# Optimization experiments

Measured on AMD Instinct MI355X. Metric: run time of the kernel, lower is better.

The kernel has to match this reference:

```python
import jax, jax.numpy as jnp
import numpy as np

D_MODEL = 1024
N_HEADS = 16
D_HEAD = D_MODEL // N_HEADS
RANK = 256
N_COMPRESS = 64
N_EXPAND = 64
N_KNOWLEDGE = 4096
K_COMPRESS = 16
K_EXPAND = 8
K_KNOW = 8


def setup_inputs() -> dict:
    key = jax.random.key(0)
    ks = jax.random.split(key, 13)
    B, S = 8, 1024
    x = jax.random.normal(ks[0], (B, S, D_MODEL), dtype=jnp.float32)
    u = jax.random.uniform(ks[1], (B, S), dtype=jnp.float32)
    importance = u / jnp.sum(u, axis=-1, keepdims=True)  # token importance weights
    s = 0.02
    compress_w = jax.random.normal(ks[2], (N_COMPRESS, D_MODEL)) * s
    expQ_w = jax.random.normal(ks[3], (N_EXPAND, D_MODEL)) * s
    expK_w = jax.random.normal(ks[4], (N_EXPAND, D_MODEL)) * s
    expV_w = jax.random.normal(ks[5], (N_EXPAND, D_MODEL)) * s
    memory_w = jax.random.normal(ks[6], (N_COMPRESS, D_MODEL)) * s
    compress_neurons = jax.random.normal(ks[7], (N_COMPRESS, D_MODEL, RANK)) / jnp.sqrt(D_MODEL)
    expand_pool = jax.random.normal(ks[8], (N_EXPAND, RANK, D_MODEL)) / jnp.sqrt(RANK)
    knowledge_K = jax.random.normal(ks[9], (N_KNOWLEDGE, RANK)) * s
    knowledge_V = jax.random.normal(ks[10], (N_KNOWLEDGE, D_MODEL)) * s
    Wo = jax.random.normal(ks[11], (D_MODEL, D_MODEL)) / jnp.sqrt(D_MODEL)
    return dict(x=x, importance=importance, compress_w=compress_w, expQ_w=expQ_w,
                expK_w=expK_w, expV_w=expV_w, memory_w=memory_w,
                compress_neurons=compress_neurons, expand_pool=expand_pool,
                knowledge_K=knowledge_K, knowledge_V=knowledge_V, Wo=Wo)


def _route(x, importance, w_lin, k):
    # softmax router pref [B,S,N], importance-weighted sum -> [B,N], renorm, top-k renorm
    pref = jax.nn.softmax(jnp.einsum('bsd,nd->bsn', x, w_lin), axis=-1)
    w = jnp.einsum('bs,bsn->bn', importance, pref)
    w = w / (jnp.sum(w, axis=-1, keepdims=True) + 1e-8)
    tw, ti = jax.lax.top_k(w, k)
    tw = tw / (jnp.sum(tw, axis=-1, keepdims=True) + 1e-8)
    return tw, ti


def _forward(x, importance, compress_w, expQ_w, expK_w, expV_w, memory_w,
             compress_neurons, expand_pool, knowledge_K, knowledge_V, Wo):
    B, S, D = x.shape
    # ---- attention routing ----
    cw, ci = _route(x, importance, compress_w, K_COMPRESS)
    shared_c = jnp.einsum('bk,bkdr->bdr', cw, compress_neurons[ci])  # [B,D,R]
    h = jnp.einsum('bsd,bdr->bsr', x, shared_c)                      # [B,S,R]

    def expand(w_lin):
        ew, ei = _route(x, importance, w_lin, K_EXPAND)
        shared = jnp.einsum('bk,bkrd->brd', ew, expand_pool[ei])     # [B,R,D]
        return jnp.einsum('bsr,brd->bsd', h, shared)                 # [B,S,D]

    Q, K, V = expand(expQ_w), expand(expK_w), expand(expV_w)
    Qh = Q.reshape(B, S, N_HEADS, D_HEAD).transpose(0, 2, 1, 3)
    Kh = K.reshape(B, S, N_HEADS, D_HEAD).transpose(0, 2, 1, 3)
    Vh = V.reshape(B, S, N_HEADS, D_HEAD).transpose(0, 2, 1, 3)
    scores = jnp.einsum('bhqd,bhkd->bhqk', Qh, Kh) / jnp.sqrt(jnp.float32(D_HEAD))
    causal = jnp.tril(jnp.ones((S, S), dtype=bool))
    scores = jnp.where(causal, scores, jnp.float32(-1e30))
    attn = jax.nn.softmax(scores, axis=-1)
    out = jnp.einsum('bhqk,bhkd->bhqd', attn, Vh)
    out = out.transpose(0, 2, 1, 3).reshape(B, S, D)
    attn_out = jnp.einsum('bsd,ed->bse', out, Wo)

    # ---- memory routing (knowledge lookup) ----
    mw, mi = _route(x, importance, memory_w, K_COMPRESS)
    shared_m = jnp.einsum('bk,bkdr->bdr', mw, compress_neurons[mi])
    hm = jnp.einsum('bsd,bdr->bsr', x, shared_m)                     # [B,S,R]
    kscores = jnp.einsum('bsr,nr->bsn', hm, knowledge_K) / jnp.sqrt(jnp.float32(RANK))
    top_s, top_i = jax.lax.top_k(kscores, K_KNOW)                    # [B,S,k]
    p = jax.nn.softmax(top_s, axis=-1)
    mem_out = jnp.einsum('bsk,bskd->bsd', p, knowledge_V[top_i])

    return attn_out + mem_out


def reference(x, importance, compress_w, expQ_w, expK_w, expV_w, memory_w,
              compress_neurons, expand_pool, knowledge_K, knowledge_V, Wo):
    return _forward(x, importance, compress_w, expQ_w, expK_w, expV_w, memory_w,
                    compress_neurons, expand_pool, knowledge_K, knowledge_V, Wo)
```

## Files before the change

kernel.cpp:

```cpp
#include <hip/hip_runtime.h>

#define Bn   8
#define Sn   1024
#define Dn   1024
#define Rn   256
#define NHn  16
#define DHn  64
#define NKn  4096
#define TOK  (Bn*Sn)
#define EPE  (Dn*Rn)

typedef __attribute__((ext_vector_type(8))) short short8;
typedef __attribute__((ext_vector_type(4))) float f32x4;
typedef __attribute__((ext_vector_type(4))) unsigned short ushort4v;

__device__ inline unsigned short f2bf(float f) {
    union { float f; unsigned u; } v; v.f = f;
    unsigned r = v.u + 0x7fffu + ((v.u >> 16) & 1u);
    return (unsigned short)(r >> 16);
}
__device__ inline float bf2f(unsigned short h) {
    union { unsigned u; float f; } v; v.u = ((unsigned)h) << 16;
    return v.f;
}
__device__ inline void f2bf_split(float f, unsigned short& hi, unsigned short& lo) {
    hi = f2bf(f);
    lo = f2bf(f - bf2f(hi));
}

__global__ __launch_bounds__(256) void convert_split(
    const float* __restrict__ src, unsigned short* __restrict__ hi,
    unsigned short* __restrict__ lo, long long n4)
{
    long long i = (long long)blockIdx.x*256 + threadIdx.x;
    if (i >= n4) return;
    float4 f = *(const float4*)&src[i*4];
    float vals[4] = {f.x, f.y, f.z, f.w};
    ushort4v h, l;
#pragma unroll
    for (int e = 0; e < 4; ++e) {
        unsigned short a, b2; f2bf_split(vals[e], a, b2);
        h[e] = a; l[e] = b2;
    }
    *(ushort4v*)&hi[i*4] = h;
    *(ushort4v*)&lo[i*4] = l;
}

__global__ __launch_bounds__(256) void gemm_pre(
    const unsigned short* __restrict__ Ahi, const unsigned short* __restrict__ Alo,
    const unsigned short* __restrict__ Bhi, const unsigned short* __restrict__ Blo,
    void* __restrict__ C0, void* __restrict__ C1,
    int M, int N, int K, long long sA, long long sB, long long sC,
    float alpha, int bTrans, int passes, int outMode)
{
    Ahi += (size_t)blockIdx.z * sA;
    if (Alo) Alo += (size_t)blockIdx.z * sA;
    Bhi += (size_t)blockIdx.z * sB;
    if (Blo) Blo += (size_t)blockIdx.z * sB;
    __shared__ __align__(16) unsigned short AsH[128][40];
    __shared__ __align__(16) unsigned short AsL[128][40];
    __shared__ __align__(16) unsigned short BsH[64][40];
    __shared__ __align__(16) unsigned short BsL[64][40];
    int tid = threadIdx.x;
    int wave = tid >> 6, lane = tid & 63;
    int lr = lane & 15, lg = lane >> 4;
    int wm = (wave >> 1)*64, wn = (wave & 1)*32;
    int row0 = blockIdx.y*128, col0 = blockIdx.x*64;

    f32x4 acc[4][2];
#pragma unroll
    for (int i = 0; i < 4; ++i)
#pragma unroll
        for (int j = 0; j < 2; ++j) acc[i][j] = (f32x4){0.f,0.f,0.f,0.f};

    for (int k0 = 0; k0 < K; k0 += 32) {
        __syncthreads();
#pragma unroll
        for (int g = 0; g < 2; ++g) {
            int idx = tid + g*256;
            int m2 = idx >> 2, kk = (idx & 3)*8;
            size_t so = (size_t)(row0 + m2)*K + k0 + kk;
            *(short8*)&AsH[m2][kk] = *(const short8*)&Ahi[so];
            if (passes >= 2) *(short8*)&AsL[m2][kk] = *(const short8*)&Alo[so];
        }
        if (!bTrans) {
            int n2 = tid >> 2, kk = (tid & 3)*8;
            size_t so = (size_t)(col0 + n2)*K + k0 + kk;
            *(short8*)&BsH[n2][kk] = *(const short8*)&Bhi[so];
            if (passes >= 3) *(short8*)&BsL[n2][kk] = *(const short8*)&Blo[so];
        } else {
            int kk = tid >> 3, n0 = (tid & 7)*8;
            size_t so = (size_t)(k0 + kk)*N + col0 + n0;
            short8 wh = *(const short8*)&Bhi[so];
#pragma unroll
            for (int e = 0; e < 8; ++e) BsH[n0+e][kk] = (unsigned short)wh[e];
            if (passes >= 3) {
                short8 wl = *(const short8*)&Blo[so];
#pragma unroll
                for (int e = 0; e < 8; ++e) BsL[n0+e][kk] = (unsigned short)wl[e];
            }
        }
        __syncthreads();
        short8 afH[4], bfH[2];
#pragma unroll
        for (int i = 0; i < 4; ++i) afH[i] = *(const short8*)&AsH[wm + i*16 + lr][lg*8];
#pragma unroll
        for (int j = 0; j < 2; ++j) bfH[j] = *(const short8*)&BsH[wn + j*16 + lr][lg*8];
#pragma unroll
        for (int i = 0; i < 4; ++i)
#pragma unroll
            for (int j = 0; j < 2; ++j)
                acc[i][j] = __builtin_amdgcn_mfma_f32_16x16x32_bf16(afH[i], bfH[j], acc[i][j], 0, 0, 0);
        if (passes >= 2) {
            short8 afL[4];
#pragma unroll
            for (int i = 0; i < 4; ++i) afL[i] = *(const short8*)&AsL[wm + i*16 + lr][lg*8];
#pragma unroll
            for (int i = 0; i < 4; ++i)
#pragma unroll
                for (int j = 0; j < 2; ++j)
                    acc[i][j] = __builtin_amdgcn_mfma_f32_16x16x32_bf16(afL[i], bfH[j], acc[i][j], 0, 0, 0);
        }
        if (passes >= 3) {
            short8 bfL[2];
#pragma unroll
            for (int j = 0; j < 2; ++j) bfL[j] = *(const short8*)&BsL[wn + j*16 + lr][lg*8];
#pragma unroll
            for (int i = 0; i < 4; ++i)
#pragma unroll
                for (int j = 0; j < 2; ++j)
                    acc[i][j] = __builtin_amdgcn_mfma_f32_16x16x32_bf16(afH[i], bfL[j], acc[i][j], 0, 0, 0);
        }
    }
#pragma unroll
    for (int i = 0; i < 4; ++i)
#pragma unroll
        for (int j = 0; j < 2; ++j)
#pragma unroll
            for (int r = 0; r < 4; ++r) {
                size_t eo = (size_t)(row0 + wm + i*16 + lg*4 + r)*N + col0 + wn + j*16 + lr;
                float val = acc[i][j][r] * alpha;
                if (outMode == 0) {
                    ((float*)C0 + (size_t)blockIdx.z*sC)[eo] = val;
                } else if (outMode == 1) {
                    ((unsigned short*)C0 + (size_t)blockIdx.z*sC)[eo] = f2bf(val);
                } else if (outMode == 2) {
                    unsigned short h, l; f2bf_split(val, h, l);
                    ((unsigned short*)C0 + (size_t)blockIdx.z*sC)[eo] = h;
                    ((unsigned short*)C1 + (size_t)blockIdx.z*sC)[eo] = l;
                } else {
                    ((float*)C0 + (size_t)blockIdx.z*sC)[eo] = val;
                    ((unsigned short*)C1 + (size_t)blockIdx.z*sC)[eo] = f2bf(val);
                }
            }
}

__global__ __launch_bounds__(256) void router_post(
    const float* __restrict__ logits, const float* __restrict__ imp,
    float* __restrict__ partial)
{
    int blk = blockIdx.x;
    int chunk = blk & 3, b = (blk >> 2) & 7, r = blk >> 5;
    int tid = threadIdx.x, lane = tid & 63, wv = tid >> 6;
    float acc = 0.f;
    for (int i = wv; i < 256; i += 4) {
        int t = b*1024 + chunk*256 + i;
        float lgv = logits[(size_t)t*320 + r*64 + lane];
        float mx = lgv;
        for (int off = 32; off >= 1; off >>= 1) mx = fmaxf(mx, __shfl_xor(mx, off));
        float e = __expf(lgv - mx);
        float s = e;
        for (int off = 32; off >= 1; off >>= 1) s += __shfl_xor(s, off);
        acc += imp[t] * e / s;
    }
    __shared__ float red[4][64];
    red[wv][lane] = acc;
    __syncthreads();
    if (tid < 64)
        partial[((size_t)(r*8 + b)*4 + chunk)*64 + tid]
            = red[0][tid] + red[1][tid] + red[2][tid] + red[3][tid];
}

__global__ void topk_router(const float* __restrict__ partial,
                            float* __restrict__ tw, int* __restrict__ ti)
{
    int rb = blockIdx.x;
    int r  = rb >> 3;
    int lane = threadIdx.x;
    float v = partial[((size_t)rb*4 + 0)*64 + lane] + partial[((size_t)rb*4 + 1)*64 + lane]
            + partial[((size_t)rb*4 + 2)*64 + lane] + partial[((size_t)rb*4 + 3)*64 + lane];
    float s = v;
    for (int off = 32; off >= 1; off >>= 1) s += __shfl_xor(s, off);
    v = v / (s + 1e-8f);
    int k = (r == 0 || r == 4) ? 16 : 8;
    __shared__ float tv[16];
    __shared__ int   tix[16];
    float cur = v;
    for (int it = 0; it < k; ++it) {
        float bv = cur; int bi = lane;
        for (int off = 32; off >= 1; off >>= 1) {
            float ov = __shfl_xor(bv, off);
            int   oi = __shfl_xor(bi, off);
            if (ov > bv || (ov == bv && oi < bi)) { bv = ov; bi = oi; }
        }
        if (bi == lane) cur = -1e30f;
        if (lane == 0) { tv[it] = bv; tix[it] = bi; }
    }
    __syncthreads();
    float s2 = 0.f;
    for (int i = 0; i < k; ++i) s2 += tv[i];
    float inv = 1.f / (s2 + 1e-8f);
    if (lane < k) {
        tw[(size_t)rb*16 + lane] = tv[lane] * inv;
        ti[(size_t)rb*16 + lane] = tix[lane];
    }
}

__global__ __launch_bounds__(256) void combine_split(
    const float* __restrict__ table, const float* __restrict__ tw,
    const int* __restrict__ ti, unsigned short* __restrict__ outhi,
    unsigned short* __restrict__ outlo, int k)
{
    int b = blockIdx.y;
    size_t e = ((size_t)blockIdx.x*256 + threadIdx.x)*4;
    float4 acc = {0.f, 0.f, 0.f, 0.f};
    for (int i = 0; i < k; ++i) {
        float w = tw[b*16 + i];
        int  idx = ti[b*16 + i];
        float4 t = *(const float4*)&table[(size_t)idx*EPE + e];
        acc.x += w*t.x; acc.y += w*t.y; acc.z += w*t.z; acc.w += w*t.w;
    }
    float vals[4] = {acc.x, acc.y, acc.z, acc.w};
    ushort4v h, l;
#pragma unroll
    for (int i = 0; i < 4; ++i) {
        unsigned short a, b2; f2bf_split(vals[i], a, b2);
        h[i] = a; l[i] = b2;
    }
    *(ushort4v*)&outhi[(size_t)b*EPE + e] = h;
    *(ushort4v*)&outlo[(size_t)b*EPE + e] = l;
}

#define PADK 72

__global__ __launch_bounds__(256, 4) void attn_mfma_kernel(
    const unsigned short* __restrict__ Q, const unsigned short* __restrict__ K,
    const unsigned short* __restrict__ V,
    unsigned short* __restrict__ Ohi, unsigned short* __restrict__ Olo)
{
    int aa = blockIdx.x;
    int hh = blockIdx.y, b = blockIdx.z;
    int qt0 = aa, qt1 = 15 - aa;
    int tid  = threadIdx.x;
    int wave = tid >> 6, lane = tid & 63;
    int lr = lane & 15, lg = lane >> 4;

    __shared__ __align__(16) unsigned short Kt[64][PADK];
    __shared__ __align__(16) unsigned short Vt[64][PADK];
    __shared__ __align__(16) unsigned short Pt[64][PADK];

    const unsigned short* Qr0 =
        Q + ((size_t)b*Sn + (size_t)qt0*64 + wave*16 + lr)*Dn + hh*64;
    const unsigned short* Qr1 =
        Q + ((size_t)b*Sn + (size_t)qt1*64 + wave*16 + lr)*Dn + hh*64;
    short8 q0a = *(const short8*)&Qr0[lg*8];
    short8 q0b = *(const short8*)&Qr0[32 + lg*8];
    short8 q1a = *(const short8*)&Qr1[lg*8];
    short8 q1b = *(const short8*)&Qr1[32 + lg*8];

    f32x4 o0[4], o1[4];
    float m0[4], l0[4], m1[4], l1[4];
#pragma unroll
    for (int ct = 0; ct < 4; ++ct) {
        o0[ct] = (f32x4){0.f,0.f,0.f,0.f};
        o1[ct] = (f32x4){0.f,0.f,0.f,0.f};
    }
#pragma unroll
    for (int r = 0; r < 4; ++r) {
        m0[r] = -1e30f; l0[r] = 0.f;
        m1[r] = -1e30f; l1[r] = 0.f;
    }

    auto process = [&](short8 qa, short8 qb, f32x4 (&o)[4],
                       float (&m)[4], float (&l)[4], int qt, int kt) {
        f32x4 s[4];
#pragma unroll
        for (int ct = 0; ct < 4; ++ct) {
            s[ct] = (f32x4){0.f,0.f,0.f,0.f};
            short8 k0 = *(const short8*)&Kt[ct*16 + lr][lg*8];
            short8 k1 = *(const short8*)&Kt[ct*16 + lr][32 + lg*8];
            s[ct] = __builtin_amdgcn_mfma_f32_16x16x32_bf16(qa, k0, s[ct], 0, 0, 0);
            s[ct] = __builtin_amdgcn_mfma_f32_16x16x32_bf16(qb, k1, s[ct], 0, 0, 0);
        }
        float mx[4] = {-1e30f,-1e30f,-1e30f,-1e30f};
        int qg0 = qt*64 + wave*16 + lg*4;
#pragma unroll
        for (int ct = 0; ct < 4; ++ct) {
            int kvg = kt*64 + ct*16 + lr;
#pragma unroll
            for (int r = 0; r < 4; ++r) {
                float v = s[ct][r] * 0.125f;
                if (kt == qt && kvg > qg0 + r) v = -1e30f;
                s[ct][r] = v;
                mx[r] = fmaxf(mx[r], v);
            }
        }
#pragma unroll
        for (int r = 0; r < 4; ++r) {
            mx[r] = fmaxf(mx[r], __shfl_xor(mx[r], 1));
            mx[r] = fmaxf(mx[r], __shfl_xor(mx[r], 2));
            mx[r] = fmaxf(mx[r], __shfl_xor(mx[r], 4));
            mx[r] = fmaxf(mx[r], __shfl_xor(mx[r], 8));
        }
        float corr[4], ps[4] = {0.f,0.f,0.f,0.f};
#pragma unroll
        for (int r = 0; r < 4; ++r) {
            float mn = fmaxf(m[r], mx[r]);
            corr[r] = __expf(m[r] - mn);
            m[r] = mn;
        }
#pragma unroll
        for (int ct = 0; ct < 4; ++ct)
#pragma unroll
            for (int r = 0; r < 4; ++r) {
                float e = __expf(s[ct][r] - m[r]);
                s[ct][r] = e;
                ps[r] += e;
            }
#pragma unroll
        for (int r = 0; r < 4; ++r) {
            ps[r] += __shfl_xor(ps[r], 1);
            ps[r] += __shfl_xor(ps[r], 2);
            ps[r] += __shfl_xor(ps[r], 4);
            ps[r] += __shfl_xor(ps[r], 8);
            l[r] = l[r]*corr[r] + ps[r];
#pragma unroll
            for (int ct = 0; ct < 4; ++ct) o[ct][r] *= corr[r];
        }
#pragma unroll
        for (int ct = 0; ct < 4; ++ct)
#pragma unroll
            for (int r = 0; r < 4; ++r)
                Pt[wave*16 + lg*4 + r][ct*16 + lr] = f2bf(s[ct][r]);
        short8 pa0 = *(const short8*)&Pt[wave*16 + lr][lg*8];
        short8 pa1 = *(const short8*)&Pt[wave*16 + lr][32 + lg*8];
#pragma unroll
        for (int ct = 0; ct < 4; ++ct) {
            short8 v0 = *(const short8*)&Vt[ct*16 + lr][lg*8];
            short8 v1 = *(const short8*)&Vt[ct*16 + lr][32 + lg*8];
            o[ct] = __builtin_amdgcn_mfma_f32_16x16x32_bf16(pa0, v0, o[ct], 0, 0, 0);
            o[ct] = __builtin_amdgcn_mfma_f32_16x16x32_bf16(pa1, v1, o[ct], 0, 0, 0);
        }
    };

    for (int kt = 0; kt <= qt1; ++kt) {
        __syncthreads();
        const unsigned short* Kb = K + ((size_t)b*Sn + (size_t)kt*64)*Dn + hh*64;
        const unsigned short* Vb = V + ((size_t)b*Sn + (size_t)kt*64)*Dn + hh*64;
#pragma unroll
        for (int it2 = 0; it2 < 2; ++it2) {
            int idx = tid + it2*256;
            int kv = idx >> 3, d0 = (idx & 7)*8;
            *(short8*)&Kt[kv][d0] = *(const short8*)&Kb[(size_t)kv*Dn + d0];
        }
#pragma unroll
        for (int it2 = 0; it2 < 2; ++it2) {
            int idx = tid + it2*256;
            int kv = idx & 63, d0 = (idx >> 6)*8;
            short8 w = *(const short8*)&Vb[(size_t)kv*Dn + d0];
#pragma unroll
            for (int e = 0; e < 8; ++e) Vt[d0+e][kv] = (unsigned short)w[e];
        }
        __syncthreads();

        if (kt <= qt0) process(q0a, q0b, o0, m0, l0, qt0, kt);
        process(q1a, q1b, o1, m1, l1, qt1, kt);
    }

    {
        size_t base = ((size_t)b*Sn + (size_t)qt0*64 + wave*16 + lg*4)*Dn + hh*64 + lr;
#pragma unroll
        for (int r = 0; r < 4; ++r) {
            float inv = 1.f / l0[r];
#pragma unroll
            for (int ct = 0; ct < 4; ++ct) {
                float val = o0[ct][r] * inv;
                unsigned short h, lo2; f2bf_split(val, h, lo2);
                Ohi[base + (size_t)r*Dn + ct*16] = h;
                Olo[base + (size_t)r*Dn + ct*16] = lo2;
            }
        }
    }
    {
        size_t base = ((size_t)b*Sn + (size_t)qt1*64 + wave*16 + lg*4)*Dn + hh*64 + lr;
#pragma unroll
        for (int r = 0; r < 4; ++r) {
            float inv = 1.f / l1[r];
#pragma unroll
            for (int ct = 0; ct < 4; ++ct) {
                float val = o1[ct][r] * inv;
                unsigned short h, lo2; f2bf_split(val, h, lo2);
                Ohi[base + (size_t)r*Dn + ct*16] = h;
                Olo[base + (size_t)r*Dn + ct*16] = lo2;
            }
        }
    }
}

__global__ __launch_bounds__(256) void mem_topk_wave(
    const float* __restrict__ ksc,
    const float* __restrict__ hm,
    const float* __restrict__ kK,
    const float* __restrict__ kV,
    float* __restrict__ out, int tok0)
{
    int wave = threadIdx.x >> 6, lane = threadIdx.x & 63;
    int t = blockIdx.x*4 + wave;
    const float* row = ksc + (size_t)t*NKn;

    float v[64];
    float lmax = -3e38f;
#pragma unroll
    for (int j4 = 0; j4 < 16; ++j4) {
        float4 f = *(const float4*)&row[lane*64 + j4*4];
        v[j4*4+0]=f.x; v[j4*4+1]=f.y; v[j4*4+2]=f.z; v[j4*4+3]=f.w;
        lmax = fmaxf(lmax, fmaxf(fmaxf(f.x, f.y), fmaxf(f.z, f.w)));
    }

    float sv = lmax;
#pragma unroll
    for (int k = 2; k <= 64; k <<= 1) {
#pragma unroll
        for (int j = k >> 1; j >= 1; j >>= 1) {
            float ov = __shfl_xor(sv, j);
            bool keepLarger = (((lane & j) == 0) == ((lane & k) == 0));
            float mx = fmaxf(sv, ov), mn = fminf(sv, ov);
            sv = keepLarger ? mx : mn;
        }
    }
    float T = __shfl(sv, 15);

    __shared__ float s_cv[4][64];
    __shared__ int   s_cix[4][64];
    __shared__ float s_cs[4][16];
    __shared__ int   s_tix[4][16];

    int cnt = 0;
#pragma unroll
    for (int j = 0; j < 64; ++j) cnt += (v[j] >= T) ? 1 : 0;
    int pre = cnt;
#pragma unroll
    for (int off2 = 1; off2 < 64; off2 <<= 1) {
        int og = __shfl_up(pre, off2);
        if (lane >= off2) pre += og;
    }
    int C = __shfl(pre, 63);
    int base = pre - cnt;

    if (C <= 64) {
        int pos = base;
#pragma unroll
        for (int j = 0; j < 64; ++j) {
            if (v[j] >= T) {
                s_cv[wave][pos] = v[j];
                s_cix[wave][pos] = lane*64 + j;
                ++pos;
            }
        }
        float cv2 = (lane < C) ? s_cv[wave][lane] : -3e38f;
        int   cix = (lane < C) ? s_cix[wave][lane] : 0x7fffffff;
#pragma unroll
        for (int k = 2; k <= 64; k <<= 1) {
#pragma unroll
            for (int j = k >> 1; j >= 1; j >>= 1) {
                float ov = __shfl_xor(cv2, j);
                int   oi = __shfl_xor(cix, j);
                bool amLarger = (cv2 > ov) || (cv2 == ov && cix < oi);
                bool keepLarger = (((lane & j) == 0) == ((lane & k) == 0));
                if (amLarger != keepLarger) { cv2 = ov; cix = oi; }
            }
        }
        if (lane < 16) s_tix[wave][lane] = cix;
    } else {
        for (int it = 0; it < 16; ++it) {
            float bv = -3e38f; int bi = 0x7fffffff;
#pragma unroll
            for (int j = 0; j < 64; ++j) {
                int n = lane*64 + j;
                if (v[j] > bv || (v[j] == bv && n < bi)) { bv = v[j]; bi = n; }
            }
#pragma unroll
            for (int off2 = 32; off2 >= 1; off2 >>= 1) {
                float ov = __shfl_xor(bv, off2);
                int   oi = __shfl_xor(bi, off2);
                if (ov > bv || (ov == bv && oi < bi)) { bv = ov; bi = oi; }
            }
            if (lane == 0) s_tix[wave][it] = bi;
#pragma unroll
            for (int j = 0; j < 64; ++j)
                if (lane*64 + j == bi) v[j] = -3e38f;
        }
    }

    int c = lane >> 2, q = lane & 3;
    int kidx = s_tix[wave][c];
    const float* kr = kK + (size_t)kidx*Rn;
    const float* hr = hm + (size_t)(tok0 + t)*Rn;
    float d = 0.f;
#pragma unroll
    for (int j4 = 0; j4 < 16; ++j4) {
        float4 a  = *(const float4*)&hr[q*64 + j4*4];
        float4 bb = *(const float4*)&kr[q*64 + j4*4];
        d += a.x*bb.x + a.y*bb.y + a.z*bb.z + a.w*bb.w;
    }
    d += __shfl_xor(d, 1);
    d += __shfl_xor(d, 2);
    if (q == 0) s_cs[wave][c] = d * 0.0625f;

    float cv = (lane < 16) ? s_cs[wave][lane] : -3e38f;
    int   ck = (lane < 16) ? s_tix[wave][lane] : 0x7fffffff;
    float sv8[8]; int si[8];
#pragma unroll
    for (int it = 0; it < 8; ++it) {
        float bv = cv; int bk = ck;
#pragma unroll
        for (int off2 = 32; off2 >= 1; off2 >>= 1) {
            float ov = __shfl_xor(bv, off2);
            int   ok = __shfl_xor(bk, off2);
            if (ov > bv || (ov == bv && ok < bk)) { bv = ov; bk = ok; }
        }
        sv8[it] = bv; si[it] = bk;
        if (ck == bk) cv = -3e38f;
    }

    float mxv = sv8[0];
#pragma unroll
    for (int kx = 1; kx < 8; ++kx) mxv = fmaxf(mxv, sv8[kx]);
    float p[8]; float sum = 0.f;
#pragma unroll
    for (int kx = 0; kx < 8; ++kx) { p[kx] = __expf(sv8[kx] - mxv); sum += p[kx]; }
    float invs = 1.f / sum;
    float4 acc0 = {0,0,0,0}, acc1 = {0,0,0,0}, acc2 = {0,0,0,0}, acc3 = {0,0,0,0};
#pragma unroll
    for (int kx = 0; kx < 8; ++kx) {
        float pk = p[kx]*invs;
        const float* vp = kV + (size_t)si[kx]*Dn + lane*16;
        float4 v0 = *(const float4*)(vp + 0);
        float4 v1 = *(const float4*)(vp + 4);
        float4 v2 = *(const float4*)(vp + 8);
        float4 v3 = *(const float4*)(vp + 12);
        acc0.x += pk*v0.x; acc0.y += pk*v0.y; acc0.z += pk*v0.z; acc0.w += pk*v0.w;
        acc1.x += pk*v1.x; acc1.y += pk*v1.y; acc1.z += pk*v1.z; acc1.w += pk*v1.w;
        acc2.x += pk*v2.x; acc2.y += pk*v2.y; acc2.z += pk*v2.z; acc2.w += pk*v2.w;
        acc3.x += pk*v3.x; acc3.y += pk*v3.y; acc3.z += pk*v3.z; acc3.w += pk*v3.w;
    }
    float* op = out + (size_t)(tok0 + t)*Dn + lane*16;
    float4 c0 = *(const float4*)(op + 0);
    float4 c1 = *(const float4*)(op + 4);
    float4 c2 = *(const float4*)(op + 8);
    float4 c3 = *(const float4*)(op + 12);
    c0.x+=acc0.x; c0.y+=acc0.y; c0.z+=acc0.z; c0.w+=acc0.w;
    c1.x+=acc1.x; c1.y+=acc1.y; c1.z+=acc1.z; c1.w+=acc1.w;
    c2.x+=acc2.x; c2.y+=acc2.y; c2.z+=acc2.z; c2.w+=acc2.w;
    c3.x+=acc3.x; c3.y+=acc3.y; c3.z+=acc3.z; c3.w+=acc3.w;
    *(float4*)(op + 0)  = c0;
    *(float4*)(op + 4)  = c1;
    *(float4*)(op + 8)  = c2;
    *(float4*)(op + 12) = c3;
}

extern "C" void kernel_launch(void* const* d_in, const int* in_sizes, int n_in,
                              void* d_out, int out_size, void* d_ws, size_t ws_size,
                              hipStream_t stream)
{
    const float* x          = (const float*)d_in[0];
    const float* imp        = (const float*)d_in[1];
    const float* compress_w = (const float*)d_in[2];
    const float* expQ_w     = (const float*)d_in[3];
    const float* expK_w     = (const float*)d_in[4];
    const float* expV_w     = (const float*)d_in[5];
    const float* memory_w   = (const float*)d_in[6];
    const float* neurons    = (const float*)d_in[7];
    const float* pool       = (const float*)d_in[8];
    const float* kK         = (const float*)d_in[9];
    const float* kV         = (const float*)d_in[10];
    const float* Wo         = (const float*)d_in[11];
    float* out = (float*)d_out;

    char* ws = (char*)d_ws;
    size_t off = 0;
    auto alloc = [&](size_t bytes) {
        size_t o = off; off = (off + bytes + 255) & ~(size_t)255; return (void*)(ws + o);
    };
    typedef unsigned short ush;
    ush* xqh    = (ush*)alloc((size_t)TOK*Dn*2);
    ush* xql    = (ush*)alloc((size_t)TOK*Dn*2);
    ush* wcatqh = (ush*)alloc((size_t)320*Dn*2);
    ush* wcatql = (ush*)alloc((size_t)320*Dn*2);
    ush* Woqh   = (ush*)alloc((size_t)Dn*Dn*2);
    ush* Woql   = (ush*)alloc((size_t)Dn*Dn*2);
    ush* kKqh   = (ush*)alloc((size_t)NKn*Rn*2);
    ush* kKql   = (ush*)alloc((size_t)NKn*Rn*2);
    float* logits  = (float*)alloc((size_t)TOK*320*4);
    float* partial = (float*)alloc((size_t)40*4*64*4);
    float* tw      = (float*)alloc((size_t)5*Bn*16*4);
    int*   ti      = (int*)  alloc((size_t)5*Bn*16*4);
    ush* shcqh = (ush*)alloc((size_t)Bn*EPE*2);
    ush* shcql = (ush*)alloc((size_t)Bn*EPE*2);
    ush* shmqh = (ush*)alloc((size_t)Bn*EPE*2);
    ush* shmql = (ush*)alloc((size_t)Bn*EPE*2);
    ush* sQqh  = (ush*)alloc((size_t)Bn*EPE*2);
    ush* sQql  = (ush*)alloc((size_t)Bn*EPE*2);
    ush* sKqh  = (ush*)alloc((size_t)Bn*EPE*2);
    ush* sKql  = (ush*)alloc((size_t)Bn*EPE*2);
    ush* sVqh  = (ush*)alloc((size_t)Bn*EPE*2);
    ush* sVql  = (ush*)alloc((size_t)Bn*EPE*2);
    ush* hqh   = (ush*)alloc((size_t)TOK*Rn*2);
    ush* hql   = (ush*)alloc((size_t)TOK*Rn*2);
    float* hm  = (float*)alloc((size_t)TOK*Rn*4);
    ush* hmqh  = (ush*)alloc((size_t)TOK*Rn*2);
    ush* Qb16  = (ush*)alloc((size_t)TOK*Dn*2);
    ush* Kb16  = (ush*)alloc((size_t)TOK*Dn*2);
    ush* Vb16  = (ush*)alloc((size_t)TOK*Dn*2);
    ush* Obqh  = (ush*)alloc((size_t)TOK*Dn*2);
    ush* Obql  = (ush*)alloc((size_t)TOK*Dn*2);
    float* ksc = (float*)Qb16;
    (void)ws_size; (void)in_sizes; (void)n_in; (void)out_size;

    convert_split<<<(TOK*Dn/4 + 255)/256, 256, 0, stream>>>(x, xqh, xql, (long long)TOK*Dn/4);
    convert_split<<<64, 256, 0, stream>>>(compress_w, wcatqh + 0*64*Dn, wcatql + 0*64*Dn, (long long)64*Dn/4);
    convert_split<<<64, 256, 0, stream>>>(expQ_w,     wcatqh + 1*64*Dn, wcatql + 1*64*Dn, (long long)64*Dn/4);
    convert_split<<<64, 256, 0, stream>>>(expK_w,     wcatqh + 2*64*Dn, wcatql + 2*64*Dn, (long long)64*Dn/4);
    convert_split<<<64, 256, 0, stream>>>(expV_w,     wcatqh + 3*64*Dn, wcatql + 3*64*Dn, (long long)64*Dn/4);
    convert_split<<<64, 256, 0, stream>>>(memory_w,   wcatqh + 4*64*Dn, wcatql + 4*64*Dn, (long long)64*Dn/4);
    convert_split<<<(Dn*Dn/4 + 255)/256, 256, 0, stream>>>(Wo, Woqh, Woql, (long long)Dn*Dn/4);
    convert_split<<<(NKn*Rn/4 + 255)/256, 256, 0, stream>>>(kK, kKqh, kKql, (long long)NKn*Rn/4);

    gemm_pre<<<dim3(5, 64, 1), 256, 0, stream>>>(
        xqh, xql, wcatqh, wcatql, logits, nullptr,
        TOK, 320, Dn, 0LL, 0LL, 0LL, 1.f, 0 , 3, 0);
    router_post<<<160, 256, 0, stream>>>(logits, imp, partial);
    topk_router<<<40, 64, 0, stream>>>(partial, tw, ti);

    dim3 cgrid(EPE/1024, Bn);
    combine_split<<<cgrid, 256, 0, stream>>>(neurons, tw + 0*128, ti + 0*128, shcqh, shcql, 16);
    combine_split<<<cgrid, 256, 0, stream>>>(pool,    tw + 1*128, ti + 1*128, sQqh,  sQql,  8);
    combine_split<<<cgrid, 256, 0, stream>>>(pool,    tw + 2*128, ti + 2*128, sKqh,  sKql,  8);
    combine_split<<<cgrid, 256, 0, stream>>>(pool,    tw + 3*128, ti + 3*128, sVqh,  sVql,  8);
    combine_split<<<cgrid, 256, 0, stream>>>(neurons, tw + 4*128, ti + 4*128, shmqh, shmql, 16);

    gemm_pre<<<dim3(Rn/64, Sn/128, Bn), 256, 0, stream>>>(
        xqh, xql, shcqh, shcql, hqh, hql,
        Sn, Rn, Dn, (long long)Sn*Dn, (long long)EPE, (long long)Sn*Rn, 1.f, 1 , 3, 2);
    gemm_pre<<<dim3(Rn/64, Sn/128, Bn), 256, 0, stream>>>(
        xqh, xql, shmqh, shmql, hm, hmqh,
        Sn, Rn, Dn, (long long)Sn*Dn, (long long)EPE, (long long)Sn*Rn, 1.f, 1, 3, 3);

    gemm_pre<<<dim3(Dn/64, Sn/128, Bn), 256, 0, stream>>>(
        hqh, hql, sQqh, sQql, Qb16, nullptr,
        Sn, Dn, Rn, (long long)Sn*Rn, (long long)EPE, (long long)Sn*Dn, 1.f, 1, 3, 1);
    gemm_pre<<<dim3(Dn/64, Sn/128, Bn), 256, 0, stream>>>(
        hqh, hql, sKqh, sKql, Kb16, nullptr,
        Sn, Dn, Rn, (long long)Sn*Rn, (long long)EPE, (long long)Sn*Dn, 1.f, 1, 3, 1);
    gemm_pre<<<dim3(Dn/64, Sn/128, Bn), 256, 0, stream>>>(
        hqh, hql, sVqh, sVql, Vb16, nullptr,
        Sn, Dn, Rn, (long long)Sn*Rn, (long long)EPE, (long long)Sn*Dn, 1.f, 1, 3, 1);

    attn_mfma_kernel<<<dim3(8, NHn, Bn), 256, 0, stream>>>(Qb16, Kb16, Vb16, Obqh, Obql);

    gemm_pre<<<dim3(Dn/64, TOK/128, 1), 256, 0, stream>>>(
        Obqh, Obql, Woqh, Woql, out, nullptr,
        TOK, Dn, Dn, 0LL, 0LL, 0LL, 1.f, 0 , 2, 0);

    for (int c = 0; c < 2; ++c) {
        gemm_pre<<<dim3(NKn/64, 4096/128, 1), 256, 0, stream>>>(
            hmqh + (size_t)c*4096*Rn, nullptr, kKqh, nullptr, ksc, nullptr,
            4096, NKn, Rn, 0LL, 0LL, 0LL, 0.0625f, 0 , 1, 0);
        mem_topk_wave<<<1024, 256, 0, stream>>>(ksc, hm, kK, kV, out, c*4096);
    }
}
```

Before: 743.0 us.

## Fuse conversions and batched GEMMs into concatenated QKV and h/hm launches

Merges the eight conversion launches into two kernels. It concatenates the combined Q/K/V expansion matrices into one [R,3072] operand so a single GEMM writes an interleaved QKV buffer, which attention then reads with a 3072 stride. The h and hm projections are fused into one 64x64-tile GEMM that writes split outputs, and the router GEMM uses the smaller tile for more blocks. Knowledge scores are now stored as bf16 instead of fp32, halving that traffic at the cost of precision in the memory top-k selection.

```diff
diff --git a/kernel.cpp b/kernel.cpp
--- a/kernel.cpp
+++ b/kernel.cpp
@@ -9,46 +9,68 @@
 #define NKn  4096
 #define TOK  (Bn*Sn)
 #define EPE  (Dn*Rn)
+#define TDN  3072
 
 typedef __attribute__((ext_vector_type(8))) short short8;
 typedef __attribute__((ext_vector_type(4))) float f32x4;
 typedef __attribute__((ext_vector_type(4))) unsigned short ushort4v;
-
-__device__ inline unsigned short f2bf(float f) {
+typedef unsigned short ush;
+
+__device__ inline ush f2bf(float f) {
     union { float f; unsigned u; } v; v.f = f;
     unsigned r = v.u + 0x7fffu + ((v.u >> 16) & 1u);
-    return (unsigned short)(r >> 16);
-}
-__device__ inline float bf2f(unsigned short h) {
+    return (ush)(r >> 16);
+}
+__device__ inline float bf2f(ush h) {
     union { unsigned u; float f; } v; v.u = ((unsigned)h) << 16;
     return v.f;
 }
-__device__ inline void f2bf_split(float f, unsigned short& hi, unsigned short& lo) {
+__device__ inline void f2bf_split(float f, ush& hi, ush& lo) {
     hi = f2bf(f);
     lo = f2bf(f - bf2f(hi));
 }
 
-__global__ __launch_bounds__(256) void convert_split(
-    const float* __restrict__ src, unsigned short* __restrict__ hi,
-    unsigned short* __restrict__ lo, long long n4)
+__global__ __launch_bounds__(256) void convert3(
+    const float* __restrict__ s0, ush* __restrict__ h0, ush* __restrict__ l0, long long n40,
+    const float* __restrict__ s1, ush* __restrict__ h1, ush* __restrict__ l1, long long n41,
+    const float* __restrict__ s2, ush* __restrict__ h2, ush* __restrict__ l2, long long n42)
 {
     long long i = (long long)blockIdx.x*256 + threadIdx.x;
-    if (i >= n4) return;
-    float4 f = *(const float4*)&src[i*4];
+    const float* s; ush* h; ush* l;
+    if (i < n40) { s = s0; h = h0; l = l0; }
+    else if (i < n40 + n41) { i -= n40; s = s1; h = h1; l = l1; }
+    else { i -= n40 + n41; if (i >= n42) return; s = s2; h = h2; l = l2; }
+    float4 f = *(const float4*)&s[i*4];
     float vals[4] = {f.x, f.y, f.z, f.w};
-    ushort4v h, l;
-#pragma unroll
-    for (int e = 0; e < 4; ++e) {
-        unsigned short a, b2; f2bf_split(vals[e], a, b2);
-        h[e] = a; l[e] = b2;
-    }
-    *(ushort4v*)&hi[i*4] = h;
-    *(ushort4v*)&lo[i*4] = l;
+    ushort4v hv, lv;
+#pragma unroll
+    for (int e = 0; e < 4; ++e) { ush a, b2; f2bf_split(vals[e], a, b2); hv[e] = a; lv[e] = b2; }
+    *(ushort4v*)&h[i*4] = hv;
+    *(ushort4v*)&l[i*4] = lv;
+}
+
+__global__ __launch_bounds__(256) void convert_w5(
+    const float* __restrict__ w0, const float* __restrict__ w1,
+    const float* __restrict__ w2, const float* __restrict__ w3,
+    const float* __restrict__ w4, ush* __restrict__ hi, ush* __restrict__ lo)
+{
+    int y = blockIdx.y;
+    const float* srcs[5] = {w0, w1, w2, w3, w4};
+    const float* s = srcs[y];
+    long long i = (long long)blockIdx.x*256 + threadIdx.x;
+    float4 f = *(const float4*)&s[i*4];
+    float vals[4] = {f.x, f.y, f.z, f.w};
+    ushort4v hv, lv;
+#pragma unroll
+    for (int e = 0; e < 4; ++e) { ush a, b2; f2bf_split(vals[e], a, b2); hv[e] = a; lv[e] = b2; }
+    size_t dst = (size_t)y*64*Dn + i*4;
+    *(ushort4v*)&hi[dst] = hv;
+    *(ushort4v*)&lo[dst] = lv;
 }
 
 __global__ __launch_bounds__(256) void gemm_pre(
-    const unsigned short* __restrict__ Ahi, const unsigned short* __restrict__ Alo,
-    const unsigned short* __restrict__ Bhi, const unsigned short* __restrict__ Blo,
+    const ush* __restrict__ Ahi, const ush* __restrict__ Alo,
+    const ush* __restrict__ Bhi, const ush* __restrict__ Blo,
     void* __restrict__ C0, void* __restrict__ C1,
     int M, int N, int K, long long sA, long long sB, long long sC,
     float alpha, int bTrans, int passes, int outMode)
@@ -57,10 +79,10 @@
     if (Alo) Alo += (size_t)blockIdx.z * sA;
     Bhi += (size_t)blockIdx.z * sB;
     if (Blo) Blo += (size_t)blockIdx.z * sB;
-    __shared__ __align__(16) unsigned short AsH[128][40];
-    __shared__ __align__(16) unsigned short AsL[128][40];
-    __shared__ __align__(16) unsigned short BsH[64][40];
-    __shared__ __align__(16) unsigned short BsL[64][40];
+    __shared__ __align__(16) ush AsH[128][40];
+    __shared__ __align__(16) ush AsL[128][40];
+    __shared__ __align__(16) ush BsH[64][40];
+    __shared__ __align__(16) ush BsL[64][40];
     int tid = threadIdx.x;
     int wave = tid >> 6, lane = tid & 63;
     int lr = lane & 15, lg = lane >> 4;
@@ -93,11 +115,11 @@
             size_t so = (size_t)(k0 + kk)*N + col0 + n0;
             short8 wh = *(const short8*)&Bhi[so];
 #pragma unroll
-            for (int e = 0; e < 8; ++e) BsH[n0+e][kk] = (unsigned short)wh[e];
+            for (int e = 0; e < 8; ++e) BsH[n0+e][kk] = (ush)wh[e];
             if (passes >= 3) {
                 short8 wl = *(const short8*)&Blo[so];
 #pragma unroll
-                for (int e = 0; e < 8; ++e) BsL[n0+e][kk] = (unsigned short)wl[e];
+                for (int e = 0; e < 8; ++e) BsL[n0+e][kk] = (ush)wl[e];
             }
         }
         __syncthreads();
@@ -143,14 +165,123 @@
                 if (outMode == 0) {
                     ((float*)C0 + (size_t)blockIdx.z*sC)[eo] = val;
                 } else if (outMode == 1) {
-                    ((unsigned short*)C0 + (size_t)blockIdx.z*sC)[eo] = f2bf(val);
-                } else if (outMode == 2) {
-                    unsigned short h, l; f2bf_split(val, h, l);
-                    ((unsigned short*)C0 + (size_t)blockIdx.z*sC)[eo] = h;
-                    ((unsigned short*)C1 + (size_t)blockIdx.z*sC)[eo] = l;
+                    ((ush*)C0 + (size_t)blockIdx.z*sC)[eo] = f2bf(val);
                 } else {
-                    ((float*)C0 + (size_t)blockIdx.z*sC)[eo] = val;
-                    ((unsigned short*)C1 + (size_t)blockIdx.z*sC)[eo] = f2bf(val);
+                    ush h, l; f2bf_split(val, h, l);
+                    ((ush*)C0 + (size_t)blockIdx.z*sC)[eo] = h;
+                    ((ush*)C1 + (size_t)blockIdx.z*sC)[eo] = l;
+                }
+            }
+}
+
+__global__ __launch_bounds__(256) void gemm64(
+    const ush* __restrict__ Ahi, const ush* __restrict__ Alo,
+    const ush* __restrict__ Bhi, const ush* __restrict__ Blo,
+    void* __restrict__ C0, void* __restrict__ C1,
+    void* __restrict__ C2, void* __restrict__ C3,
+    int N, int K, long long sA, long long sB, long long sCL, long long sCR,
+    float alpha, int bTrans, int passes, int mode)
+{
+    Ahi += (size_t)blockIdx.z * sA;
+    if (Alo) Alo += (size_t)blockIdx.z * sA;
+    Bhi += (size_t)blockIdx.z * sB;
+    if (Blo) Blo += (size_t)blockIdx.z * sB;
+    __shared__ __align__(16) ush AsH[64][40];
+    __shared__ __align__(16) ush AsL[64][40];
+    __shared__ __align__(16) ush BsH[64][40];
+    __shared__ __align__(16) ush BsL[64][40];
+    int tid = threadIdx.x;
+    int wave = tid >> 6, lane = tid & 63;
+    int lr = lane & 15, lg = lane >> 4;
+    int wm = (wave >> 1)*32, wn = (wave & 1)*32;
+    int row0 = blockIdx.y*64, col0 = blockIdx.x*64;
+
+    f32x4 acc[2][2];
+#pragma unroll
+    for (int i = 0; i < 2; ++i)
+#pragma unroll
+        for (int j = 0; j < 2; ++j) acc[i][j] = (f32x4){0.f,0.f,0.f,0.f};
+
+    for (int k0 = 0; k0 < K; k0 += 32) {
+        __syncthreads();
+        {
+            int m2 = tid >> 2, kk = (tid & 3)*8;
+            size_t so = (size_t)(row0 + m2)*K + k0 + kk;
+            *(short8*)&AsH[m2][kk] = *(const short8*)&Ahi[so];
+            if (passes >= 2) *(short8*)&AsL[m2][kk] = *(const short8*)&Alo[so];
+        }
+        if (!bTrans) {
+            int n2 = tid >> 2, kk = (tid & 3)*8;
+            size_t so = (size_t)(col0 + n2)*K + k0 + kk;
+            *(short8*)&BsH[n2][kk] = *(const short8*)&Bhi[so];
+            if (passes >= 3) *(short8*)&BsL[n2][kk] = *(const short8*)&Blo[so];
+        } else {
+            int kk = tid >> 3, n0 = (tid & 7)*8;
+            size_t so = (size_t)(k0 + kk)*N + col0 + n0;
+            short8 wh = *(const short8*)&Bhi[so];
+#pragma unroll
+            for (int e = 0; e < 8; ++e) BsH[n0+e][kk] = (ush)wh[e];
+            if (passes >= 3) {
+                short8 wl = *(const short8*)&Blo[so];
+#pragma unroll
+                for (int e = 0; e < 8; ++e) BsL[n0+e][kk] = (ush)wl[e];
+            }
+        }
+        __syncthreads();
+        short8 afH[2], bfH[2];
+#pragma unroll
+        for (int i = 0; i < 2; ++i) afH[i] = *(const short8*)&AsH[wm + i*16 + lr][lg*8];
+#pragma unroll
+        for (int j = 0; j < 2; ++j) bfH[j] = *(const short8*)&BsH[wn + j*16 + lr][lg*8];
+#pragma unroll
+        for (int i = 0; i < 2; ++i)
+#pragma unroll
+            for (int j = 0; j < 2; ++j)
+                acc[i][j] = __builtin_amdgcn_mfma_f32_16x16x32_bf16(afH[i], bfH[j], acc[i][j], 0, 0, 0);
+        if (passes >= 2) {
+            short8 afL[2];
+#pragma unroll
+            for (int i = 0; i < 2; ++i) afL[i] = *(const short8*)&AsL[wm + i*16 + lr][lg*8];
+#pragma unroll
+            for (int i = 0; i < 2; ++i)
+#pragma unroll
+                for (int j = 0; j < 2; ++j)
+                    acc[i][j] = __builtin_amdgcn_mfma_f32_16x16x32_bf16(afL[i], bfH[j], acc[i][j], 0, 0, 0);
+        }
+        if (passes >= 3) {
+            short8 bfL[2];
+#pragma unroll
+            for (int j = 0; j < 2; ++j) bfL[j] = *(const short8*)&BsL[wn + j*16 + lr][lg*8];
+#pragma unroll
+            for (int i = 0; i < 2; ++i)
+#pragma unroll
+                for (int j = 0; j < 2; ++j)
+                    acc[i][j] = __builtin_amdgcn_mfma_f32_16x16x32_bf16(afH[i], bfL[j], acc[i][j], 0, 0, 0);
+        }
+    }
+    int Nh = N >> 1;
+#pragma unroll
+    for (int i = 0; i < 2; ++i)
+#pragma unroll
+        for (int j = 0; j < 2; ++j)
+#pragma unroll
+            for (int r = 0; r < 4; ++r) {
+                int grow = row0 + wm + i*16 + lg*4 + r;
+                int gcol = col0 + wn + j*16 + lr;
+                float val = acc[i][j][r] * alpha;
+                if (mode == 0) {
+                    ((float*)C0 + (size_t)blockIdx.z*sCL)[(size_t)grow*N + gcol] = val;
+                } else {
+                    if (gcol < Nh) {
+                        ush h, l; f2bf_split(val, h, l);
+                        size_t eo = (size_t)blockIdx.z*sCL + (size_t)grow*Nh + gcol;
+                        ((ush*)C0)[eo] = h;
+                        ((ush*)C1)[eo] = l;
+                    } else {
+                        size_t eo = (size_t)blockIdx.z*sCR + (size_t)grow*Nh + (gcol - Nh);
+                        ((float*)C2)[eo] = val;
+                        ((ush*)C3)[eo] = f2bf(val);
+                    }
                 }
             }
 }
@@ -218,8 +349,9 @@
 
 __global__ __launch_bounds__(256) void combine_split(
     const float* __restrict__ table, const float* __restrict__ tw,
-    const int* __restrict__ ti, unsigned short* __restrict__ outhi,
-    unsigned short* __restrict__ outlo, int k)
+    const int* __restrict__ ti, ush* __restrict__ outhi,
+    ush* __restrict__ outlo, int k, int nInner, int rowStride, int colOff,
+    long long sOut)
 {
     int b = blockIdx.y;
     size_t e = ((size_t)blockIdx.x*256 + threadIdx.x)*4;
@@ -234,19 +366,20 @@
     ushort4v h, l;
 #pragma unroll
     for (int i = 0; i < 4; ++i) {
-        unsigned short a, b2; f2bf_split(vals[i], a, b2);
+        ush a, b2; f2bf_split(vals[i], a, b2);
         h[i] = a; l[i] = b2;
     }
-    *(ushort4v*)&outhi[(size_t)b*EPE + e] = h;
-    *(ushort4v*)&outlo[(size_t)b*EPE + e] = l;
+    int row = (int)(e / nInner), col = (int)(e % nInner);
+    size_t dst = (size_t)b*sOut + (size_t)row*rowStride + colOff + col;
+    *(ushort4v*)&outhi[dst] = h;
+    *(ushort4v*)&outlo[dst] = l;
 }
 
 #define PADK 72
 
 __global__ __launch_bounds__(256, 4) void attn_mfma_kernel(
-    const unsigned short* __restrict__ Q, const unsigned short* __restrict__ K,
-    const unsigned short* __restrict__ V,
-    unsigned short* __restrict__ Ohi, unsigned short* __restrict__ Olo)
+    const ush* __restrict__ QKV,
+    ush* __restrict__ Ohi, ush* __restrict__ Olo)
 {
     int aa = blockIdx.x;
     int hh = blockIdx.y, b = blockIdx.z;
@@ -255,14 +388,12 @@
     int wave = tid >> 6, lane = tid & 63;
     int lr = lane & 15, lg = lane >> 4;
 
-    __shared__ __align__(16) unsigned short Kt[64][PADK];
-    __shared__ __align__(16) unsigned short Vt[64][PADK];
-    __shared__ __align__(16) unsigned short Pt[64][PADK];
-
-    const unsigned short* Qr0 =
-        Q + ((size_t)b*Sn + (size_t)qt0*64 + wave*16 + lr)*Dn + hh*64;
-    const unsigned short* Qr1 =
-        Q + ((size_t)b*Sn + (size_t)qt1*64 + wave*16 + lr)*Dn + hh*64;
+    __shared__ __align__(16) ush Kt[64][PADK];
+    __shared__ __align__(16) ush Vt[64][PADK];
+    __shared__ __align__(16) ush Pt[64][PADK];
+
+    const ush* Qr0 = QKV + ((size_t)b*Sn + (size_t)qt0*64 + wave*16 + lr)*TDN + hh*64;
+    const ush* Qr1 = QKV + ((size_t)b*Sn + (size_t)qt1*64 + wave*16 + lr)*TDN + hh*64;
     short8 q0a = *(const short8*)&Qr0[lg*8];
     short8 q0b = *(const short8*)&Qr0[32 + lg*8];
     short8 q1a = *(const short8*)&Qr1[lg*8];
@@ -355,21 +486,21 @@
 
     for (int kt = 0; kt <= qt1; ++kt) {
         __syncthreads();
-        const unsigned short* Kb = K + ((size_t)b*Sn + (size_t)kt*64)*Dn + hh*64;
-        const unsigned short* Vb = V + ((size_t)b*Sn + (size_t)kt*64)*Dn + hh*64;
+        const ush* Kb = QKV + ((size_t)b*Sn + (size_t)kt*64)*TDN + 1024 + hh*64;
+        const ush* Vb = QKV + ((size_t)b*Sn + (size_t)kt*64)*TDN + 2048 + hh*64;
 #pragma unroll
         for (int it2 = 0; it2 < 2; ++it2) {
             int idx = tid + it2*256;
             int kv = idx >> 3, d0 = (idx & 7)*8;
-            *(short8*)&Kt[kv][d0] = *(const short8*)&Kb[(size_t)kv*Dn + d0];
+            *(short8*)&Kt[kv][d0] = *(const short8*)&Kb[(size_t)kv*TDN + d0];
         }
 #pragma unroll
         for (int it2 = 0; it2 < 2; ++it2) {
             int idx = tid + it2*256;
             int kv = idx & 63, d0 = (idx >> 6)*8;
-            short8 w = *(const short8*)&Vb[(size_t)kv*Dn + d0];
-#pragma unroll
-            for (int e = 0; e < 8; ++e) Vt[d0+e][kv] = (unsigned short)w[e];
+            short8 w = *(const short8*)&Vb[(size_t)kv*TDN + d0];
+#pragma unroll
+            for (int e = 0; e < 8; ++e) Vt[d0+e][kv] = (ush)w[e];
         }
         __syncthreads();
 
@@ -385,7 +516,7 @@
 #pragma unroll
             for (int ct = 0; ct < 4; ++ct) {
                 float val = o0[ct][r] * inv;
-                unsigned short h, lo2; f2bf_split(val, h, lo2);
+                ush h, lo2; f2bf_split(val, h, lo2);
                 Ohi[base + (size_t)r*Dn + ct*16] = h;
                 Olo[base + (size_t)r*Dn + ct*16] = lo2;
             }
@@ -399,7 +530,7 @@
 #pragma unroll
             for (int ct = 0; ct < 4; ++ct) {
                 float val = o1[ct][r] * inv;
-                unsigned short h, lo2; f2bf_split(val, h, lo2);
+                ush h, lo2; f2bf_split(val, h, lo2);
                 Ohi[base + (size_t)r*Dn + ct*16] = h;
                 Olo[base + (size_t)r*Dn + ct*16] = lo2;
             }
@@ -408,7 +539,7 @@
 }
 
 __global__ __launch_bounds__(256) void mem_topk_wave(
-    const float* __restrict__ ksc,
+    const ush* __restrict__ ksc,
     const float* __restrict__ hm,
     const float* __restrict__ kK,
     const float* __restrict__ kV,
@@ -416,15 +547,19 @@
 {
     int wave = threadIdx.x >> 6, lane = threadIdx.x & 63;
     int t = blockIdx.x*4 + wave;
-    const float* row = ksc + (size_t)t*NKn;
+    const ush* row = ksc + (size_t)t*NKn;
 
     float v[64];
     float lmax = -3e38f;
 #pragma unroll
-    for (int j4 = 0; j4 < 16; ++j4) {
-        float4 f = *(const float4*)&row[lane*64 + j4*4];
-        v[j4*4+0]=f.x; v[j4*4+1]=f.y; v[j4*4+2]=f.z; v[j4*4+3]=f.w;
-        lmax = fmaxf(lmax, fmaxf(fmaxf(f.x, f.y), fmaxf(f.z, f.w)));
+    for (int j8 = 0; j8 < 8; ++j8) {
+        short8 w = *(const short8*)&row[lane*64 + j8*8];
+#pragma unroll
+        for (int e = 0; e < 8; ++e) {
+            float f = bf2f((ush)w[e]);
+            v[j8*8+e] = f;
+            lmax = fmaxf(lmax, f);
+        }
     }
 
     float sv = lmax;
@@ -592,7 +727,6 @@
     auto alloc = [&](size_t bytes) {
         size_t o = off; off = (off + bytes + 255) & ~(size_t)255; return (void*)(ws + o);
     };
-    typedef unsigned short ush;
     ush* xqh    = (ush*)alloc((size_t)TOK*Dn*2);
     ush* xql    = (ush*)alloc((size_t)TOK*Dn*2);
     ush* wcatqh = (ush*)alloc((size_t)320*Dn*2);
@@ -605,68 +739,56 @@
     float* partial = (float*)alloc((size_t)40*4*64*4);
     float* tw      = (float*)alloc((size_t)5*Bn*16*4);
     int*   ti      = (int*)  alloc((size_t)5*Bn*16*4);
-    ush* shcqh = (ush*)alloc((size_t)Bn*EPE*2);
-    ush* shcql = (ush*)alloc((size_t)Bn*EPE*2);
-    ush* shmqh = (ush*)alloc((size_t)Bn*EPE*2);
-    ush* shmql = (ush*)alloc((size_t)Bn*EPE*2);
-    ush* sQqh  = (ush*)alloc((size_t)Bn*EPE*2);
-    ush* sQql  = (ush*)alloc((size_t)Bn*EPE*2);
-    ush* sKqh  = (ush*)alloc((size_t)Bn*EPE*2);
-    ush* sKql  = (ush*)alloc((size_t)Bn*EPE*2);
-    ush* sVqh  = (ush*)alloc((size_t)Bn*EPE*2);
-    ush* sVql  = (ush*)alloc((size_t)Bn*EPE*2);
+    ush* hhmBh = (ush*)alloc((size_t)Bn*2*EPE*2);
+    ush* hhmBl = (ush*)alloc((size_t)Bn*2*EPE*2);
+    ush* qkvBh = (ush*)alloc((size_t)Bn*3*EPE*2);
+    ush* qkvBl = (ush*)alloc((size_t)Bn*3*EPE*2);
     ush* hqh   = (ush*)alloc((size_t)TOK*Rn*2);
     ush* hql   = (ush*)alloc((size_t)TOK*Rn*2);
     float* hm  = (float*)alloc((size_t)TOK*Rn*4);
     ush* hmqh  = (ush*)alloc((size_t)TOK*Rn*2);
-    ush* Qb16  = (ush*)alloc((size_t)TOK*Dn*2);
-    ush* Kb16  = (ush*)alloc((size_t)TOK*Dn*2);
-    ush* Vb16  = (ush*)alloc((size_t)TOK*Dn*2);
+    ush* QKVb  = (ush*)alloc((size_t)TOK*TDN*2);
     ush* Obqh  = (ush*)alloc((size_t)TOK*Dn*2);
     ush* Obql  = (ush*)alloc((size_t)TOK*Dn*2);
-    float* ksc = (float*)Qb16;
+    ush* ksc = QKVb;
     (void)ws_size; (void)in_sizes; (void)n_in; (void)out_size;
 
-    convert_split<<<(TOK*Dn/4 + 255)/256, 256, 0, stream>>>(x, xqh, xql, (long long)TOK*Dn/4);
-    convert_split<<<64, 256, 0, stream>>>(compress_w, wcatqh + 0*64*Dn, wcatql + 0*64*Dn, (long long)64*Dn/4);
-    convert_split<<<64, 256, 0, stream>>>(expQ_w,     wcatqh + 1*64*Dn, wcatql + 1*64*Dn, (long long)64*Dn/4);
-    convert_split<<<64, 256, 0, stream>>>(expK_w,     wcatqh + 2*64*Dn, wcatql + 2*64*Dn, (long long)64*Dn/4);
-    convert_split<<<64, 256, 0, stream>>>(expV_w,     wcatqh + 3*64*Dn, wcatql + 3*64*Dn, (long long)64*Dn/4);
-    convert_split<<<64, 256, 0, stream>>>(memory_w,   wcatqh + 4*64*Dn, wcatql + 4*64*Dn, (long long)64*Dn/4);
-    convert_split<<<(Dn*Dn/4 + 255)/256, 256, 0, stream>>>(Wo, Woqh, Woql, (long long)Dn*Dn/4);
-    convert_split<<<(NKn*Rn/4 + 255)/256, 256, 0, stream>>>(kK, kKqh, kKql, (long long)NKn*Rn/4);
-
-    gemm_pre<<<dim3(5, 64, 1), 256, 0, stream>>>(
-        xqh, xql, wcatqh, wcatql, logits, nullptr,
-        TOK, 320, Dn, 0LL, 0LL, 0LL, 1.f, 0 , 3, 0);
+    convert3<<<10240, 256, 0, stream>>>(
+        x, xqh, xql, (long long)TOK*Dn/4,
+        Wo, Woqh, Woql, (long long)Dn*Dn/4,
+        kK, kKqh, kKql, (long long)NKn*Rn/4);
+    convert_w5<<<dim3(64, 5), 256, 0, stream>>>(
+        compress_w, expQ_w, expK_w, expV_w, memory_w, wcatqh, wcatql);
+
+    gemm64<<<dim3(5, 128, 1), 256, 0, stream>>>(
+        xqh, xql, wcatqh, wcatql, logits, nullptr, nullptr, nullptr,
+        320, Dn, 0LL, 0LL, 0LL, 0LL, 1.f, 0 , 3, 0);
     router_post<<<160, 256, 0, stream>>>(logits, imp, partial);
     topk_router<<<40, 64, 0, stream>>>(partial, tw, ti);
 
     dim3 cgrid(EPE/1024, Bn);
-    combine_split<<<cgrid, 256, 0, stream>>>(neurons, tw + 0*128, ti + 0*128, shcqh, shcql, 16);
-    combine_split<<<cgrid, 256, 0, stream>>>(pool,    tw + 1*128, ti + 1*128, sQqh,  sQql,  8);
-    combine_split<<<cgrid, 256, 0, stream>>>(pool,    tw + 2*128, ti + 2*128, sKqh,  sKql,  8);
-    combine_split<<<cgrid, 256, 0, stream>>>(pool,    tw + 3*128, ti + 3*128, sVqh,  sVql,  8);
-    combine_split<<<cgrid, 256, 0, stream>>>(neurons, tw + 4*128, ti + 4*128, shmqh, shmql, 16);
-
-    gemm_pre<<<dim3(Rn/64, Sn/128, Bn), 256, 0, stream>>>(
-        xqh, xql, shcqh, shcql, hqh, hql,
-        Sn, Rn, Dn, (long long)Sn*Dn, (long long)EPE, (long long)Sn*Rn, 1.f, 1 , 3, 2);
-    gemm_pre<<<dim3(Rn/64, Sn/128, Bn), 256, 0, stream>>>(
-        xqh, xql, shmqh, shmql, hm, hmqh,
-        Sn, Rn, Dn, (long long)Sn*Dn, (long long)EPE, (long long)Sn*Rn, 1.f, 1, 3, 3);
-
-    gemm_pre<<<dim3(Dn/64, Sn/128, Bn), 256, 0, stream>>>(
-        hqh, hql, sQqh, sQql, Qb16, nullptr,
-        Sn, Dn, Rn, (long long)Sn*Rn, (long long)EPE, (long long)Sn*Dn, 1.f, 1, 3, 1);
-    gemm_pre<<<dim3(Dn/64, Sn/128, Bn), 256, 0, stream>>>(
-        hqh, hql, sKqh, sKql, Kb16, nullptr,
-        Sn, Dn, Rn, (long long)Sn*Rn, (long long)EPE, (long long)Sn*Dn, 1.f, 1, 3, 1);
-    gemm_pre<<<dim3(Dn/64, Sn/128, Bn), 256, 0, stream>>>(
-        hqh, hql, sVqh, sVql, Vb16, nullptr,
-        Sn, Dn, Rn, (long long)Sn*Rn, (long long)EPE, (long long)Sn*Dn, 1.f, 1, 3, 1);
-
-    attn_mfma_kernel<<<dim3(8, NHn, Bn), 256, 0, stream>>>(Qb16, Kb16, Vb16, Obqh, Obql);
+    combine_split<<<cgrid, 256, 0, stream>>>(neurons, tw + 0*128, ti + 0*128,
+        hhmBh, hhmBl, 16, 256, 512, 0,   (long long)2*EPE);
+    combine_split<<<cgrid, 256, 0, stream>>>(neurons, tw + 4*128, ti + 4*128,
+        hhmBh, hhmBl, 16, 256, 512, 256, (long long)2*EPE);
+    combine_split<<<cgrid, 256, 0, stream>>>(pool, tw + 1*128, ti + 1*128,
+        qkvBh, qkvBl, 8, 1024, TDN, 0,    (long long)3*EPE);
+    combine_split<<<cgrid, 256, 0, stream>>>(pool, tw + 2*128, ti + 2*128,
+        qkvBh, qkvBl, 8, 1024, TDN, 1024, (long long)3*EPE);
+    combine_split<<<cgrid, 256, 0, stream>>>(pool, tw + 3*128, ti + 3*128,
+        qkvBh, qkvBl, 8, 1024, TDN, 2048, (long long)3*EPE);
+
+    gemm64<<<dim3(8, 16, Bn), 256, 0, stream>>>(
+        xqh, xql, hhmBh, hhmBl, hqh, hql, hm, hmqh,
+        512, Dn, (long long)Sn*Dn, (long long)2*EPE,
+        (long long)Sn*Rn, (long long)Sn*Rn, 1.f, 1 , 3, 1);
+
+    gemm_pre<<<dim3(TDN/64, Sn/128, Bn), 256, 0, stream>>>(
+        hqh, hql, qkvBh, qkvBl, QKVb, nullptr,
+        Sn, TDN, Rn, (long long)Sn*Rn, (long long)3*EPE, (long long)Sn*TDN,
+        1.f, 1 , 3, 1);
+
+    attn_mfma_kernel<<<dim3(8, NHn, Bn), 256, 0, stream>>>(QKVb, Obqh, Obql);
 
     gemm_pre<<<dim3(Dn/64, TOK/128, 1), 256, 0, stream>>>(
         Obqh, Obql, Woqh, Woql, out, nullptr,
@@ -675,7 +797,7 @@
     for (int c = 0; c < 2; ++c) {
         gemm_pre<<<dim3(NKn/64, 4096/128, 1), 256, 0, stream>>>(
             hmqh + (size_t)c*4096*Rn, nullptr, kKqh, nullptr, ksc, nullptr,
-            4096, NKn, Rn, 0LL, 0LL, 0LL, 0.0625f, 0 , 1, 0);
+            4096, NKn, Rn, 0LL, 0LL, 0LL, 0.0625f, 0 , 1, 1 );
         mem_topk_wave<<<1024, 256, 0, stream>>>(ksc, hm, kK, kV, out, c*4096);
     }
 }
```

Result: faster. 662.0 us (-10.9%).
